# Kernel tuning notes

Measured on AMD Instinct MI355X. Metric: run time of the kernel, lower is better.

## Reference

```python
import jax, jax.numpy as jnp
import numpy as np

FEATURE_SIZE = 1_000_000
EMB = 64
BATCH = 16384
ONEHOT = 26
MULTIHOT = 2
MH_LEN = 20
DENSE = 13
NN_IN = EMB * (ONEHOT + MULTIHOT) + DENSE  # 1805
UNITS = [1024, 512, 1]


def setup_inputs() -> dict:
    key = jax.random.key(0)
    ks = jax.random.split(key, 12)
    glorot = lambda k, shape: jax.random.normal(k, shape, jnp.float32) * np.sqrt(2.0 / (shape[0] + shape[-1])).astype(np.float32)
    return {
        "dense": jax.random.normal(ks[0], (BATCH, DENSE), jnp.float32),
        "onehot": jax.random.randint(ks[1], (BATCH, ONEHOT), 0, FEATURE_SIZE),
        "multihot": jax.random.randint(ks[2], (BATCH, MULTIHOT, MH_LEN), 0, FEATURE_SIZE),
        "fm_w": glorot(ks[3], (FEATURE_SIZE, 1)),
        "fm_emb": glorot(ks[4], (FEATURE_SIZE, EMB)),
        "w0": glorot(ks[5], (NN_IN, UNITS[0])),
        "b0": jnp.zeros((1,), jnp.float32),
        "w1": glorot(ks[6], (UNITS[0], UNITS[1])),
        "b1": jnp.zeros((1,), jnp.float32),
        "w2": glorot(ks[7], (UNITS[1], UNITS[2])),
        "b2": jnp.zeros((1,), jnp.float32),
    }


def reference(dense, onehot, multihot, fm_w, fm_emb, w0, b0, w1, b1, w2, b2):
    B = dense.shape[0]
    # Embedding gathers
    onehot_emb = fm_emb[onehot]                       # (B, 26, E)
    multihot_emb = fm_emb[multihot].mean(axis=2)      # (B, 2, L, E) -> (B, 2, E) mean combiner
    cat_emb = jnp.concatenate([onehot_emb, multihot_emb], axis=1)  # (B, 28, E)
    # FM 1st order (only onehot, as in original code)
    fm_1st = jnp.sum(fm_w[onehot], axis=1)            # (B, 1)
    # FM 2nd order: 0.5 * ((sum v)^2 - sum v^2)
    s = jnp.sum(cat_emb, axis=1)                      # (B, E)
    fm_2nd = 0.5 * (jnp.square(s) - jnp.sum(jnp.square(cat_emb), axis=1))
    fm_2nd = jnp.sum(fm_2nd, axis=1, keepdims=True)   # (B, 1)
    # Deep part (ReLU on every layer, incl. last, as in original)
    nn = jnp.concatenate([cat_emb.reshape(B, -1), dense], axis=1)  # (B, 1805)
    for w, b in ((w0, b0), (w1, b1), (w2, b2)):
        nn = jax.nn.relu(nn @ w + b)
    return jax.nn.sigmoid(fm_1st + fm_2nd + nn)       # (B, 1)
```

## Files before the change

### kernel.cpp

```cpp
#include <hip/hip_runtime.h>
#include <hip/hip_bf16.h>
#include <math.h>

typedef __attribute__((ext_vector_type(8))) short bf16x8;
typedef __attribute__((ext_vector_type(4))) float f32x4;

typedef void __attribute__((address_space(1))) gvoid_t;
typedef void __attribute__((address_space(3))) lvoid_t;

#define KP0   1856
#define NB    16384
#define OFF_X    0u
#define OFF_H0   60817408u
#define OFF_W0T  94371840u
#define OFF_W1T  98172928u
#define OFF_FM   99221504u

#define VMCNT(n) asm volatile("s_waitcnt vmcnt(" #n ")" ::: "memory")
#define LGKM0()  asm volatile("s_waitcnt lgkmcnt(0)" ::: "memory")
#define SBAR0()  __builtin_amdgcn_sched_barrier(0)

__device__ __forceinline__ float bf2f(short s) {
    return __uint_as_float(((unsigned)(unsigned short)s) << 16);
}

__device__ __forceinline__ void load_lds16(const void* g, void* l) {
    __builtin_amdgcn_global_load_lds(
        (gvoid_t*)(uintptr_t)g,
        (lvoid_t*)(unsigned)(uintptr_t)l,
        16, 0, 0);
}

__global__ __launch_bounds__(256) void transpose_w(const float* __restrict__ W,
                                                   __hip_bfloat16* __restrict__ WT,
                                                   int K, int N, int KP) {
    __shared__ float tile[32][33];
    const int k0 = blockIdx.x * 32, n0 = blockIdx.y * 32;
    const int tx = threadIdx.x, ty = threadIdx.y;
    #pragma unroll
    for (int i = 0; i < 32; i += 8) {
        int k = k0 + ty + i;
        tile[ty + i][tx] = (k < K) ? W[(size_t)k * N + (n0 + tx)] : 0.f;
    }
    __syncthreads();
    #pragma unroll
    for (int i = 0; i < 32; i += 8) {
        int n = n0 + ty + i, k = k0 + tx;
        WT[(size_t)n * KP + k] = __float2bfloat16(tile[tx][ty + i]);
    }
}

__global__ __launch_bounds__(256) void gather_fm(const float* __restrict__ dense,
                                                 const int* __restrict__ onehot,
                                                 const int* __restrict__ multihot,
                                                 const float* __restrict__ fm_w,
                                                 const float* __restrict__ fm_emb,
                                                 __hip_bfloat16* __restrict__ X,
                                                 float* __restrict__ FM) {
    const int wv = threadIdx.x >> 6, lane = threadIdx.x & 63;
    const int row = blockIdx.x * 4 + wv;
    const int oh = (lane < 26) ? onehot[row * 26 + lane] : 0;
    const int mh = (lane < 40) ? multihot[row * 40 + lane] : 0;
    const float fm1 = (lane < 26) ? fm_w[oh] : 0.f;
    __hip_bfloat16* Xr = X + (size_t)row * KP0;
    float s = 0.f, sq = 0.f;
    for (int f = 0; f < 26; ++f) {
        int idx = __shfl(oh, f);
        float v = fm_emb[(size_t)idx * 64 + lane];
        s += v; sq += v * v;
        Xr[f * 64 + lane] = __float2bfloat16(v);
    }
    #pragma unroll
    for (int h = 0; h < 2; ++h) {
        float a = 0.f;
        for (int l = 0; l < 20; ++l) {
            int idx = __shfl(mh, h * 20 + l);
            a += fm_emb[(size_t)idx * 64 + lane];
        }
        float v = a * (1.f / 20.f);
        s += v; sq += v * v;
        Xr[(26 + h) * 64 + lane] = __float2bfloat16(v);
    }
    float red = 0.5f * (s * s - sq) + fm1;
    #pragma unroll
    for (int off = 32; off; off >>= 1) red += __shfl_xor(red, off);
    if (lane == 0) FM[row] = red;
    float dv = (lane < 13) ? dense[row * 13 + lane] : 0.f;
    Xr[1792 + lane] = __float2bfloat16(dv);
}

template<int NREP>
__global__ __launch_bounds__(512, 2) void gemm_pipe(const __hip_bfloat16* __restrict__ A,
                                                    const __hip_bfloat16* __restrict__ BT,
                                                    const float* __restrict__ bias,
                                                    __hip_bfloat16* __restrict__ C,
                                                    int M, int N, int K) {
    constexpr int AB   = 256 * 144;
    constexpr int BROW = (NREP == 4) ? 144 : 160;
    constexpr int BB   = (NREP == 4) ? 256 * 144 : 128 * 160;
    constexpr int TOT  = AB + BB;
    constexpr int LOADS = TOT / 8192;
    __shared__ __align__(16) char lds[2][TOT];

    const int tid = threadIdx.x;
    const int wv = tid >> 6, lane = tid & 63;
    const int lr = lane & 15, lg = lane >> 4;
    const int wr = wv >> 2, wc = wv & 3;

    const int bid = blockIdx.x;
    const int wg = (bid & 7) * 32 + (bid >> 3);
    const int br = wg >> 2, bc = wg & 3;

    const size_t rowBytes = (size_t)K * 2;
    const char* Ab = (const char*)A + (size_t)(br * 256) * rowBytes;
    const char* Bb = (const char*)BT + (size_t)(bc * (NREP * 64)) * rowBytes;
    const int nt = K >> 6;

    auto stage_chunk = [&](int t, int i) {
        const size_t kb = (size_t)t * 128;
        const int o = i * 8192 + tid * 16;
        const char* src;
        if (o < AB) {
            int row = o / 144, c = o % 144;
            if (c >= 128) c = 0;
            src = Ab + (size_t)row * rowBytes + kb + c;
        } else {
            int ob = o - AB;
            int row = ob / BROW, c = ob % BROW;
            if (c >= 128) c = 0;
            src = Bb + (size_t)row * rowBytes + kb + c;
        }
        load_lds16(src, &lds[t & 1][i * 8192 + wv * 1024]);
    };

    f32x4 acc[8][NREP] = {};

    for (int i = 0; i < LOADS; ++i) stage_chunk(0, i);
    for (int i = 0; i < LOADS; ++i) stage_chunk(1, i);
    if constexpr (NREP == 4) VMCNT(9); else VMCNT(7);
    __builtin_amdgcn_s_barrier();
    SBAR0();

    const int aoff = (wr * 128 + lr) * 144 + lg * 16;
    const int boff = AB + (wc * (NREP * 16) + lr) * BROW + lg * 16;

    for (int t = 0; t < nt; ++t) {
        const char* L = &lds[t & 1][0];
        const bool st = (t + 2 < nt);
        bf16x8 a[4][2], b[NREP][2];

        #pragma unroll
        for (int m = 0; m < 4; ++m)
            #pragma unroll
            for (int kk = 0; kk < 2; ++kk)
                a[m][kk] = *(const bf16x8*)(L + aoff + m * 2304 + kk * 64);
        #pragma unroll
        for (int n = 0; n < 2; ++n)
            #pragma unroll
            for (int kk = 0; kk < 2; ++kk)
                b[n][kk] = *(const bf16x8*)(L + boff + n * (16 * BROW) + kk * 64);
        SBAR0();
        __builtin_amdgcn_s_barrier();
        LGKM0(); SBAR0();
        __builtin_amdgcn_s_setprio(1);
        #pragma unroll
        for (int m = 0; m < 4; ++m)
            #pragma unroll
            for (int n = 0; n < 2; ++n)
                #pragma unroll
                for (int kk = 0; kk < 2; ++kk)
                    acc[m][n] = __builtin_amdgcn_mfma_f32_16x16x32_bf16(a[m][kk], b[n][kk], acc[m][n], 0, 0, 0);
        __builtin_amdgcn_s_setprio(0);
        SBAR0();
        __builtin_amdgcn_s_barrier();

        if constexpr (NREP == 4) {
            #pragma unroll
            for (int n = 2; n < 4; ++n)
                #pragma unroll
                for (int kk = 0; kk < 2; ++kk)
                    b[n][kk] = *(const bf16x8*)(L + boff + n * (16 * BROW) + kk * 64);
            SBAR0();
            __builtin_amdgcn_s_barrier();
            LGKM0(); SBAR0();
            __builtin_amdgcn_s_setprio(1);
            #pragma unroll
            for (int m = 0; m < 4; ++m)
                #pragma unroll
                for (int n = 2; n < 4; ++n)
                    #pragma unroll
                    for (int kk = 0; kk < 2; ++kk)
                        acc[m][n] = __builtin_amdgcn_mfma_f32_16x16x32_bf16(a[m][kk], b[n][kk], acc[m][n], 0, 0, 0);
            __builtin_amdgcn_s_setprio(0);
            SBAR0();
            __builtin_amdgcn_s_barrier();
        }

        #pragma unroll
        for (int m = 0; m < 4; ++m)
            #pragma unroll
            for (int kk = 0; kk < 2; ++kk)
                a[m][kk] = *(const bf16x8*)(L + aoff + (4 + m) * 2304 + kk * 64);
        if (st) {
            if constexpr (NREP == 4) {
                stage_chunk(t + 2, 5); stage_chunk(t + 2, 6);
                stage_chunk(t + 2, 7); stage_chunk(t + 2, 8);
            } else {
                stage_chunk(t + 2, 5); stage_chunk(t + 2, 6);
            }
        }
        SBAR0();
        __builtin_amdgcn_s_barrier();
        LGKM0(); SBAR0();
        __builtin_amdgcn_s_setprio(1);
        if constexpr (NREP == 4) {
            #pragma unroll
            for (int m = 0; m < 4; ++m)
                #pragma unroll
                for (int n = 0; n < 2; ++n)
                    #pragma unroll
                    for (int kk = 0; kk < 2; ++kk)
                        acc[4 + m][n] = __builtin_amdgcn_mfma_f32_16x16x32_bf16(a[m][kk], b[n][kk], acc[4 + m][n], 0, 0, 0);
        } else {
            #pragma unroll
            for (int m = 0; m < 4; ++m)
                #pragma unroll
                for (int kk = 0; kk < 2; ++kk)
                    acc[4 + m][0] = __builtin_amdgcn_mfma_f32_16x16x32_bf16(a[m][kk], b[0][kk], acc[4 + m][0], 0, 0, 0);
        }
        __builtin_amdgcn_s_setprio(0);
        SBAR0();
        __builtin_amdgcn_s_barrier();

        if (st) {
            #pragma unroll
            for (int i = 0; i < 5; ++i) stage_chunk(t + 2, i);
        }
        SBAR0();
        __builtin_amdgcn_s_barrier();
        LGKM0(); SBAR0();
        __builtin_amdgcn_s_setprio(1);
        if constexpr (NREP == 4) {
            #pragma unroll
            for (int m = 0; m < 4; ++m)
                #pragma unroll
                for (int n = 2; n < 4; ++n)
                    #pragma unroll
                    for (int kk = 0; kk < 2; ++kk)
                        acc[4 + m][n] = __builtin_amdgcn_mfma_f32_16x16x32_bf16(a[m][kk], b[n][kk], acc[4 + m][n], 0, 0, 0);
        } else {
            #pragma unroll
            for (int m = 0; m < 4; ++m)
                #pragma unroll
                for (int kk = 0; kk < 2; ++kk)
                    acc[4 + m][1] = __builtin_amdgcn_mfma_f32_16x16x32_bf16(a[m][kk], b[1][kk], acc[4 + m][1], 0, 0, 0);
        }
        __builtin_amdgcn_s_setprio(0);
        SBAR0();
        if (t + 2 < nt) { if constexpr (NREP == 4) VMCNT(9); else VMCNT(7); }
        else if (t + 1 < nt) VMCNT(0);
        if (t + 1 < nt) __builtin_amdgcn_s_barrier();
    }

    const float bv = bias[0];
    const int rowb = br * 256 + wr * 128, colb = bc * (NREP * 64) + wc * (NREP * 16);
    #pragma unroll
    for (int m = 0; m < 8; ++m)
        #pragma unroll
        for (int n = 0; n < NREP; ++n)
            #pragma unroll
            for (int r = 0; r < 4; ++r) {
                int row = rowb + m * 16 + lg * 4 + r;
                int col = colb + n * 16 + lr;
                C[(size_t)row * N + col] = __float2bfloat16(fmaxf(acc[m][n][r] + bv, 0.f));
            }
}

__global__ __launch_bounds__(256) void final_k(const __hip_bfloat16* __restrict__ H1,
                                               const float* __restrict__ w2,
                                               const float* __restrict__ b2,
                                               const float* __restrict__ FM,
                                               float* __restrict__ out) {
    const int wv = threadIdx.x >> 6, lane = threadIdx.x & 63;
    const int row = blockIdx.x * 4 + wv;
    const bf16x8 h = *(const bf16x8*)(H1 + (size_t)row * 512 + lane * 8);
    float s = 0.f;
    #pragma unroll
    for (int j = 0; j < 8; ++j) s += bf2f(h[j]) * w2[lane * 8 + j];
    #pragma unroll
    for (int off = 32; off; off >>= 1) s += __shfl_xor(s, off);
    if (lane == 0) {
        float v = fmaxf(s + b2[0], 0.f) + FM[row];
        out[row] = 1.f / (1.f + expf(-v));
    }
}

extern "C" void kernel_launch(void* const* d_in, const int* in_sizes, int n_in,
                              void* d_out, int out_size, void* d_ws, size_t ws_size,
                              hipStream_t stream) {
    const float* dense    = (const float*)d_in[0];
    const int*   onehot   = (const int*)d_in[1];
    const int*   multihot = (const int*)d_in[2];
    const float* fm_w     = (const float*)d_in[3];
    const float* fm_emb   = (const float*)d_in[4];
    const float* w0       = (const float*)d_in[5];
    const float* b0       = (const float*)d_in[6];
    const float* w1       = (const float*)d_in[7];
    const float* b1       = (const float*)d_in[8];
    const float* w2       = (const float*)d_in[9];
    const float* b2       = (const float*)d_in[10];
    float* out = (float*)d_out;

    char* ws = (char*)d_ws;
    __hip_bfloat16* X   = (__hip_bfloat16*)(ws + OFF_X);
    __hip_bfloat16* H1  = (__hip_bfloat16*)(ws + OFF_X);
    __hip_bfloat16* H0  = (__hip_bfloat16*)(ws + OFF_H0);
    __hip_bfloat16* W0T = (__hip_bfloat16*)(ws + OFF_W0T);
    __hip_bfloat16* W1T = (__hip_bfloat16*)(ws + OFF_W1T);
    float*          FM  = (float*)(ws + OFF_FM);

    transpose_w<<<dim3(58, 32), dim3(32, 8), 0, stream>>>(w0, W0T, 1805, 1024, KP0);
    transpose_w<<<dim3(32, 16), dim3(32, 8), 0, stream>>>(w1, W1T, 1024, 512, 1024);
    gather_fm<<<NB / 4, 256, 0, stream>>>(dense, onehot, multihot, fm_w, fm_emb, X, FM);
    gemm_pipe<4><<<256, 512, 0, stream>>>(X,  W0T, b0, H0, NB, 1024, KP0);
    gemm_pipe<2><<<256, 512, 0, stream>>>(H0, W1T, b1, H1, NB, 512, 1024);
    final_k<<<NB / 4, 256, 0, stream>>>(H1, w2, b2, FM, out);
}
```

Baseline: 190.3 us.

## Swizzle GEMM LDS layout, stagger A/B prefetch, fuse prep kernels into one launch

Replaces the padded-row LDS staging in the bf16 MFMA GEMM with a dense 128-byte row layout using an XOR swizzle to avoid bank conflicts. It also reschedules loads so B for the next k-tile and A for two tiles ahead are issued in pieces between MFMA phases. The two weight transposes and the embedding gather are merged into a single launch to cut launch overhead and let them overlap. The new schedule makes the wait-count and barrier logic more intricate and shrinks LDS per buffer, which could change occupancy.

New measurement: 174.1 us. 8.5% less time.

```diff
diff --git a/kernel.cpp b/kernel.cpp
--- a/kernel.cpp
+++ b/kernel.cpp
@@ -31,12 +31,11 @@
         16, 0, 0);
 }
 
-__global__ __launch_bounds__(256) void transpose_w(const float* __restrict__ W,
-                                                   __hip_bfloat16* __restrict__ WT,
-                                                   int K, int N, int KP) {
-    __shared__ float tile[32][33];
-    const int k0 = blockIdx.x * 32, n0 = blockIdx.y * 32;
-    const int tx = threadIdx.x, ty = threadIdx.y;
+__device__ __forceinline__ void transpose_tile(const float* __restrict__ W,
+                                               __hip_bfloat16* __restrict__ WT,
+                                               int K, int N, int KP, int k0, int n0,
+                                               float (*tile)[33], int tid) {
+    const int tx = tid & 31, ty = tid >> 5;
     #pragma unroll
     for (int i = 0; i < 32; i += 8) {
         int k = k0 + ty + i;
@@ -50,15 +49,31 @@
     }
 }
 
-__global__ __launch_bounds__(256) void gather_fm(const float* __restrict__ dense,
-                                                 const int* __restrict__ onehot,
-                                                 const int* __restrict__ multihot,
-                                                 const float* __restrict__ fm_w,
-                                                 const float* __restrict__ fm_emb,
-                                                 __hip_bfloat16* __restrict__ X,
-                                                 float* __restrict__ FM) {
-    const int wv = threadIdx.x >> 6, lane = threadIdx.x & 63;
-    const int row = blockIdx.x * 4 + wv;
+__global__ __launch_bounds__(256) void prep(const float* __restrict__ dense,
+                                            const int* __restrict__ onehot,
+                                            const int* __restrict__ multihot,
+                                            const float* __restrict__ fm_w,
+                                            const float* __restrict__ fm_emb,
+                                            const float* __restrict__ w0,
+                                            const float* __restrict__ w1,
+                                            __hip_bfloat16* __restrict__ X,
+                                            float* __restrict__ FM,
+                                            __hip_bfloat16* __restrict__ W0T,
+                                            __hip_bfloat16* __restrict__ W1T) {
+    __shared__ float tile[32][33];
+    const int b = blockIdx.x, tid = threadIdx.x;
+    if (b >= 4096) {
+        if (b < 4096 + 1856) {
+            int bb = b - 4096;
+            transpose_tile(w0, W0T, 1805, 1024, KP0, (bb % 58) * 32, (bb / 58) * 32, tile, tid);
+        } else {
+            int bb = b - 5952;
+            transpose_tile(w1, W1T, 1024, 512, 1024, (bb % 32) * 32, (bb / 32) * 32, tile, tid);
+        }
+        return;
+    }
+    const int wv = tid >> 6, lane = tid & 63;
+    const int row = b * 4 + wv;
     const int oh = (lane < 26) ? onehot[row * 26 + lane] : 0;
     const int mh = (lane < 40) ? multihot[row * 40 + lane] : 0;
     const float fm1 = (lane < 26) ? fm_w[oh] : 0.f;
@@ -95,12 +110,9 @@
                                                     const float* __restrict__ bias,
                                                     __hip_bfloat16* __restrict__ C,
                                                     int M, int N, int K) {
-    constexpr int AB   = 256 * 144;
-    constexpr int BROW = (NREP == 4) ? 144 : 160;
-    constexpr int BB   = (NREP == 4) ? 256 * 144 : 128 * 160;
-    constexpr int TOT  = AB + BB;
-    constexpr int LOADS = TOT / 8192;
-    __shared__ __align__(16) char lds[2][TOT];
+    constexpr int BUFB = 32768 + NREP * 8192;
+    constexpr int NBC  = NREP;
+    __shared__ __align__(16) char lds[2][BUFB];
 
     const int tid = threadIdx.x;
     const int wv = tid >> 6, lane = tid & 63;
@@ -116,150 +128,132 @@
     const char* Bb = (const char*)BT + (size_t)(bc * (NREP * 64)) * rowBytes;
     const int nt = K >> 6;
 
-    auto stage_chunk = [&](int t, int i) {
-        const size_t kb = (size_t)t * 128;
-        const int o = i * 8192 + tid * 16;
-        const char* src;
-        if (o < AB) {
-            int row = o / 144, c = o % 144;
-            if (c >= 128) c = 0;
-            src = Ab + (size_t)row * rowBytes + kb + c;
-        } else {
-            int ob = o - AB;
-            int row = ob / BROW, c = ob % BROW;
-            if (c >= 128) c = 0;
-            src = Bb + (size_t)row * rowBytes + kb + c;
-        }
-        load_lds16(src, &lds[t & 1][i * 8192 + wv * 1024]);
+    const int srcx = ((tid & 7) ^ ((tid >> 3) & 7)) << 4;
+    auto stA = [&](int tt, int c) {
+        int gr = c * 64 + (tid >> 3);
+        load_lds16(Ab + (size_t)gr * rowBytes + (size_t)tt * 128 + srcx,
+                   &lds[tt & 1][c * 8192 + wv * 1024]);
     };
+    auto stB = [&](int tt, int c) {
+        int gr = c * 64 + (tid >> 3);
+        load_lds16(Bb + (size_t)gr * rowBytes + (size_t)tt * 128 + srcx,
+                   &lds[tt & 1][32768 + c * 8192 + wv * 1024]);
+    };
 
     f32x4 acc[8][NREP] = {};
 
-    for (int i = 0; i < LOADS; ++i) stage_chunk(0, i);
-    for (int i = 0; i < LOADS; ++i) stage_chunk(1, i);
-    if constexpr (NREP == 4) VMCNT(9); else VMCNT(7);
+    #pragma unroll
+    for (int c = 0; c < 4; ++c) stA(0, c);
+    #pragma unroll
+    for (int c = 0; c < NBC; ++c) stB(0, c);
+    #pragma unroll
+    for (int c = 0; c < 4; ++c) stA(1, c);
+    VMCNT(4);
+    SBAR0();
     __builtin_amdgcn_s_barrier();
-    SBAR0();
-
-    const int aoff = (wr * 128 + lr) * 144 + lg * 16;
-    const int boff = AB + (wc * (NREP * 16) + lr) * BROW + lg * 16;
+
+    const int xr0 = (lg ^ (lr & 7)) << 4;
+    const int xr1 = ((4 + lg) ^ (lr & 7)) << 4;
+    const int arow = (wr * 128 + lr) * 128;
+    const int brow = 32768 + (wc * (NREP * 16) + lr) * 128;
 
     for (int t = 0; t < nt; ++t) {
         const char* L = &lds[t & 1][0];
-        const bool st = (t + 2 < nt);
-        bf16x8 a[4][2], b[NREP][2];
-
+        const bool sB = (t + 1 < nt), sA = (t + 2 < nt);
+        bf16x8 a[4][2], a2[4][2], b01[2][2], b23[2][2];
+
+        #pragma unroll
+        for (int m = 0; m < 4; ++m) {
+            a[m][0] = *(const bf16x8*)(L + arow + m * 2048 + xr0);
+            a[m][1] = *(const bf16x8*)(L + arow + m * 2048 + xr1);
+        }
+        {
+            constexpr int NLO = (NREP == 4) ? 2 : 1;
+            #pragma unroll
+            for (int n = 0; n < NLO; ++n) {
+                b01[n][0] = *(const bf16x8*)(L + brow + n * 2048 + xr0);
+                b01[n][1] = *(const bf16x8*)(L + brow + n * 2048 + xr1);
+            }
+        }
+        if (sB) { stB(t + 1, 0); if constexpr (NREP == 4) stB(t + 1, 1); }
+        SBAR0();
+        __builtin_amdgcn_s_barrier();
+        LGKM0();
+        __builtin_amdgcn_s_setprio(1);
         #pragma unroll
         for (int m = 0; m < 4; ++m)
             #pragma unroll
-            for (int kk = 0; kk < 2; ++kk)
-                a[m][kk] = *(const bf16x8*)(L + aoff + m * 2304 + kk * 64);
-        #pragma unroll
-        for (int n = 0; n < 2; ++n)
-            #pragma unroll
-            for (int kk = 0; kk < 2; ++kk)
-                b[n][kk] = *(const bf16x8*)(L + boff + n * (16 * BROW) + kk * 64);
-        SBAR0();
-        __builtin_amdgcn_s_barrier();
-        LGKM0(); SBAR0();
-        __builtin_amdgcn_s_setprio(1);
-        #pragma unroll
-        for (int m = 0; m < 4; ++m)
-            #pragma unroll
-            for (int n = 0; n < 2; ++n)
+            for (int n = 0; n < ((NREP == 4) ? 2 : 1); ++n)
                 #pragma unroll
                 for (int kk = 0; kk < 2; ++kk)
-                    acc[m][n] = __builtin_amdgcn_mfma_f32_16x16x32_bf16(a[m][kk], b[n][kk], acc[m][n], 0, 0, 0);
+                    acc[m][n] = __builtin_amdgcn_mfma_f32_16x16x32_bf16(a[m][kk], b01[n][kk], acc[m][n], 0, 0, 0);
         __builtin_amdgcn_s_setprio(0);
         SBAR0();
         __builtin_amdgcn_s_barrier();
 
-        if constexpr (NREP == 4) {
-            #pragma unroll
-            for (int n = 2; n < 4; ++n)
+        #pragma unroll
+        for (int m = 0; m < 4; ++m) {
+            a2[m][0] = *(const bf16x8*)(L + arow + (4 + m) * 2048 + xr0);
+            a2[m][1] = *(const bf16x8*)(L + arow + (4 + m) * 2048 + xr1);
+        }
+        if (sB) { if constexpr (NREP == 4) { stB(t + 1, 2); stB(t + 1, 3); } else stB(t + 1, 1); }
+        SBAR0();
+        __builtin_amdgcn_s_barrier();
+        LGKM0();
+        __builtin_amdgcn_s_setprio(1);
+        #pragma unroll
+        for (int m = 0; m < 4; ++m)
+            #pragma unroll
+            for (int n = 0; n < ((NREP == 4) ? 2 : 1); ++n)
                 #pragma unroll
                 for (int kk = 0; kk < 2; ++kk)
-                    b[n][kk] = *(const bf16x8*)(L + boff + n * (16 * BROW) + kk * 64);
-            SBAR0();
-            __builtin_amdgcn_s_barrier();
-            LGKM0(); SBAR0();
-            __builtin_amdgcn_s_setprio(1);
-            #pragma unroll
-            for (int m = 0; m < 4; ++m)
-                #pragma unroll
-                for (int n = 2; n < 4; ++n)
-                    #pragma unroll
-                    for (int kk = 0; kk < 2; ++kk)
-                        acc[m][n] = __builtin_amdgcn_mfma_f32_16x16x32_bf16(a[m][kk], b[n][kk], acc[m][n], 0, 0, 0);
-            __builtin_amdgcn_s_setprio(0);
-            SBAR0();
-            __builtin_amdgcn_s_barrier();
-        }
-
+                    acc[4 + m][n] = __builtin_amdgcn_mfma_f32_16x16x32_bf16(a2[m][kk], b01[n][kk], acc[4 + m][n], 0, 0, 0);
+        __builtin_amdgcn_s_setprio(0);
+        SBAR0();
+        __builtin_amdgcn_s_barrier();
+
+        {
+            constexpr int NHI = (NREP == 4) ? 2 : 1;
+            constexpr int NO  = (NREP == 4) ? 2 : 1;
+            #pragma unroll
+            for (int n = 0; n < NHI; ++n) {
+                b23[n][0] = *(const bf16x8*)(L + brow + (NO + n) * 2048 + xr0);
+                b23[n][1] = *(const bf16x8*)(L + brow + (NO + n) * 2048 + xr1);
+            }
+        }
+        if (sA) { stA(t + 2, 0); stA(t + 2, 1); }
+        SBAR0();
+        __builtin_amdgcn_s_barrier();
+        LGKM0();
+        __builtin_amdgcn_s_setprio(1);
         #pragma unroll
         for (int m = 0; m < 4; ++m)
             #pragma unroll
-            for (int kk = 0; kk < 2; ++kk)
-                a[m][kk] = *(const bf16x8*)(L + aoff + (4 + m) * 2304 + kk * 64);
-        if (st) {
-            if constexpr (NREP == 4) {
-                stage_chunk(t + 2, 5); stage_chunk(t + 2, 6);
-                stage_chunk(t + 2, 7); stage_chunk(t + 2, 8);
-            } else {
-                stage_chunk(t + 2, 5); stage_chunk(t + 2, 6);
-            }
-        }
-        SBAR0();
-        __builtin_amdgcn_s_barrier();
-        LGKM0(); SBAR0();
-        __builtin_amdgcn_s_setprio(1);
-        if constexpr (NREP == 4) {
-            #pragma unroll
-            for (int m = 0; m < 4; ++m)
-                #pragma unroll
-                for (int n = 0; n < 2; ++n)
-                    #pragma unroll
-                    for (int kk = 0; kk < 2; ++kk)
-                        acc[4 + m][n] = __builtin_amdgcn_mfma_f32_16x16x32_bf16(a[m][kk], b[n][kk], acc[4 + m][n], 0, 0, 0);
-        } else {
-            #pragma unroll
-            for (int m = 0; m < 4; ++m)
+            for (int n = 0; n < ((NREP == 4) ? 2 : 1); ++n)
                 #pragma unroll
                 for (int kk = 0; kk < 2; ++kk)
-                    acc[4 + m][0] = __builtin_amdgcn_mfma_f32_16x16x32_bf16(a[m][kk], b[0][kk], acc[4 + m][0], 0, 0, 0);
-        }
+                    acc[m][((NREP == 4) ? 2 : 1) + n] = __builtin_amdgcn_mfma_f32_16x16x32_bf16(a[m][kk], b23[n][kk], acc[m][((NREP == 4) ? 2 : 1) + n], 0, 0, 0);
         __builtin_amdgcn_s_setprio(0);
         SBAR0();
         __builtin_amdgcn_s_barrier();
 
-        if (st) {
-            #pragma unroll
-            for (int i = 0; i < 5; ++i) stage_chunk(t + 2, i);
-        }
-        SBAR0();
-        __builtin_amdgcn_s_barrier();
-        LGKM0(); SBAR0();
+        if (sA) { stA(t + 2, 2); stA(t + 2, 3); }
+        SBAR0();
+        __builtin_amdgcn_s_barrier();
+        LGKM0();
         __builtin_amdgcn_s_setprio(1);
-        if constexpr (NREP == 4) {
-            #pragma unroll
-            for (int m = 0; m < 4; ++m)
-                #pragma unroll
-                for (int n = 2; n < 4; ++n)
-                    #pragma unroll
-                    for (int kk = 0; kk < 2; ++kk)
-                        acc[4 + m][n] = __builtin_amdgcn_mfma_f32_16x16x32_bf16(a[m][kk], b[n][kk], acc[4 + m][n], 0, 0, 0);
-        } else {
-            #pragma unroll
-            for (int m = 0; m < 4; ++m)
+        #pragma unroll
+        for (int m = 0; m < 4; ++m)
+            #pragma unroll
+            for (int n = 0; n < ((NREP == 4) ? 2 : 1); ++n)
                 #pragma unroll
                 for (int kk = 0; kk < 2; ++kk)
-                    acc[4 + m][1] = __builtin_amdgcn_mfma_f32_16x16x32_bf16(a[m][kk], b[1][kk], acc[4 + m][1], 0, 0, 0);
-        }
+                    acc[4 + m][((NREP == 4) ? 2 : 1) + n] = __builtin_amdgcn_mfma_f32_16x16x32_bf16(a2[m][kk], b23[n][kk], acc[4 + m][((NREP == 4) ? 2 : 1) + n], 0, 0, 0);
         __builtin_amdgcn_s_setprio(0);
         SBAR0();
-        if (t + 2 < nt) { if constexpr (NREP == 4) VMCNT(9); else VMCNT(7); }
-        else if (t + 1 < nt) VMCNT(0);
-        if (t + 1 < nt) __builtin_amdgcn_s_barrier();
+        if (sA)      VMCNT(4);
+        else if (sB) VMCNT(0);
+        if (sB) __builtin_amdgcn_s_barrier();
     }
 
     const float bv = bias[0];
@@ -319,9 +313,8 @@
     __hip_bfloat16* W1T = (__hip_bfloat16*)(ws + OFF_W1T);
     float*          FM  = (float*)(ws + OFF_FM);
 
-    transpose_w<<<dim3(58, 32), dim3(32, 8), 0, stream>>>(w0, W0T, 1805, 1024, KP0);
-    transpose_w<<<dim3(32, 16), dim3(32, 8), 0, stream>>>(w1, W1T, 1024, 512, 1024);
-    gather_fm<<<NB / 4, 256, 0, stream>>>(dense, onehot, multihot, fm_w, fm_emb, X, FM);
+    prep<<<6464, 256, 0, stream>>>(dense, onehot, multihot, fm_w, fm_emb, w0, w1,
+                                   X, FM, W0T, W1T);
     gemm_pipe<4><<<256, 512, 0, stream>>>(X,  W0T, b0, H0, NB, 1024, KP0);
     gemm_pipe<2><<<256, 512, 0, stream>>>(H0, W1T, b1, H1, NB, 512, 1024);
     final_k<<<NB / 4, 256, 0, stream>>>(H1, w2, b2, FM, out);
```
